# Performance work log

Measured on AMD Instinct MI355X. Metric: run time of the kernel, lower is better.

Reference implementation:

```python
import jax, jax.numpy as jnp
import numpy as np

HEADS = 16
D_MODEL = 1024
HEAD_DIM = D_MODEL // HEADS
NEG = -1e15


def setup_inputs() -> dict:
    key = jax.random.key(0)
    ks = jax.random.split(key, 13)
    B, L = 2, 2048
    scale = 1.0 / np.sqrt(D_MODEL)
    inp = {
        'q': jax.random.normal(ks[0], (B, L, D_MODEL), jnp.float32),
        'k': jax.random.normal(ks[1], (B, L, D_MODEL), jnp.float32),
        'v': jax.random.normal(ks[2], (B, L, D_MODEL), jnp.float32),
        'mask': jax.random.randint(ks[3], (B, 1, 1, L), 0, 2, jnp.int32),
        'Wq': jax.random.normal(ks[4], (D_MODEL, D_MODEL), jnp.float32) * scale,
        'bq': jax.random.normal(ks[5], (D_MODEL,), jnp.float32) * scale,
        'Wk': jax.random.normal(ks[6], (D_MODEL, D_MODEL), jnp.float32) * scale,
        'bk': jax.random.normal(ks[7], (D_MODEL,), jnp.float32) * scale,
        'Wv': jax.random.normal(ks[8], (D_MODEL, D_MODEL), jnp.float32) * scale,
        'bv': jax.random.normal(ks[9], (D_MODEL,), jnp.float32) * scale,
        'Wo': jax.random.normal(ks[10], (D_MODEL, D_MODEL), jnp.float32) * scale,
        'bo': jax.random.normal(ks[11], (D_MODEL,), jnp.float32) * scale,
    }
    return inp


def _split_heads(x):
    B, L, _ = x.shape
    return x.reshape(B, L, HEADS, HEAD_DIM).transpose(0, 2, 1, 3)  # [B,H,L,Dh]


def reference(q, k, v, mask, Wq, bq, Wk, bk, Wv, bv, Wo, bo):
    B, L, _ = q.shape
    # torch Linear: y = x @ W.T + b
    qh = _split_heads(q @ Wq.T + bq)
    kh = _split_heads(k @ Wk.T + bk)
    vh = _split_heads(v @ Wv.T + bv)
    scores = jnp.einsum('bhqd,bhkd->bhqk', qh, kh) / jnp.sqrt(jnp.float32(HEAD_DIM))
    scores = scores + mask.astype(scores.dtype) * NEG
    weights = jax.nn.softmax(scores, axis=-1)
    attn = jnp.einsum('bhqk,bhkd->bhqd', weights, vh)  # [B,H,L,Dh]
    attn = attn.transpose(0, 2, 1, 3).reshape(B, L, D_MODEL)
    return attn @ Wo.T + bo
```

## Files before the change

kernel.cpp:

```cpp
#include <hip/hip_runtime.h>
#include <stdint.h>

typedef __bf16 bf16;
typedef __attribute__((ext_vector_type(8))) __bf16 bf16x8;
typedef __attribute__((ext_vector_type(4))) __bf16 bf16x4;
typedef __attribute__((ext_vector_type(4))) float f32x4;

#define SEQ   2048
#define DM    1024
#define NH    16
#define HD    64
#define MROWS 4096

__device__ __forceinline__ void glds16(const bf16* g, bf16* l) {
  __builtin_amdgcn_global_load_lds(
      (__attribute__((address_space(1))) unsigned int*)(g),
      (__attribute__((address_space(3))) unsigned int*)(l),
      16, 0, 0);
}

static __device__ __forceinline__ bf16x8 cvt_f32x8(const float* __restrict__ p) {
  const f32x4 a = *(const f32x4*)p;
  const f32x4 b = *(const f32x4*)(p + 4);
  bf16x8 r;
  r[0] = (bf16)a[0]; r[1] = (bf16)a[1]; r[2] = (bf16)a[2]; r[3] = (bf16)a[3];
  r[4] = (bf16)b[0]; r[5] = (bf16)b[1]; r[6] = (bf16)b[2]; r[7] = (bf16)b[3];
  return r;
}

__global__ void conv_all(
    const float* __restrict__ q, const float* __restrict__ k, const float* __restrict__ v,
    const float* __restrict__ wq, const float* __restrict__ wk,
    const float* __restrict__ wv, const float* __restrict__ wo,
    bf16* __restrict__ dq, bf16* __restrict__ dk, bf16* __restrict__ dv,
    bf16* __restrict__ dwq, bf16* __restrict__ dwk, bf16* __restrict__ dwv,
    bf16* __restrict__ dwo)
{
  const size_t c = (size_t)blockIdx.x * 256 + threadIdx.x;
  const float* s; bf16* d; size_t off;
  if (c < 524288)        { s = q;  d = dq;  off = c; }
  else if (c < 1048576)  { s = k;  d = dk;  off = c - 524288; }
  else if (c < 1572864)  { s = v;  d = dv;  off = c - 1048576; }
  else if (c < 1703936)  { s = wq; d = dwq; off = c - 1572864; }
  else if (c < 1835008)  { s = wk; d = dwk; off = c - 1703936; }
  else if (c < 1966080)  { s = wv; d = dwv; off = c - 1835008; }
  else                   { s = wo; d = dwo; off = c - 1966080; }
  *(bf16x8*)(d + off * 8) = cvt_f32x8(s + off * 8);
}

__global__ __launch_bounds__(256, 4) void proj_qkv(
    const bf16* __restrict__ qb, const bf16* __restrict__ kb, const bf16* __restrict__ vb,
    const bf16* __restrict__ Wqb, const bf16* __restrict__ Wkb, const bf16* __restrict__ Wvb,
    const float* __restrict__ bq, const float* __restrict__ bk, const float* __restrict__ bv,
    bf16* __restrict__ Qh, bf16* __restrict__ Kh, bf16* __restrict__ Vt)
{
  __shared__ __align__(16) bf16 sA[128 * 64];
  __shared__ __align__(16) bf16 sB[128 * 64];

  const int z = blockIdx.z;
  const int o = (int)blockIdx.x + 8 * (int)blockIdx.y;
  const int rt = (o & 7) * 4 + ((o >> 3) & 3);
  const int ot = o >> 5;

  const bf16 *A, *B;
  const float* Bv;
  int m0, n0;
  if (z == 0)      { A = qb;  B = Wqb; Bv = bq; m0 = rt * 128; n0 = ot * 128; }
  else if (z == 1) { A = kb;  B = Wkb; Bv = bk; m0 = rt * 128; n0 = ot * 128; }
  else             { A = Wvb; B = vb;  Bv = bv; m0 = ot * 128; n0 = rt * 128; }

  const int tid  = threadIdx.x;
  const int lane = tid & 63;
  const int wv   = tid >> 6;
  const int quad = lane >> 4;
  const int colx = lane & 15;
  const int rm = (wv >> 1) * 64;
  const int rn = (wv & 1) * 64;

  f32x4 acc[4][4];
#pragma unroll
  for (int mi = 0; mi < 4; ++mi)
#pragma unroll
    for (int ni = 0; ni < 4; ++ni) {
      f32x4 zz = {0.f, 0.f, 0.f, 0.f};
      acc[mi][ni] = zz;
    }

  for (int kt = 0; kt < 16; ++kt) {
    const int k0 = kt * 64;
    __syncthreads();
#pragma unroll
    for (int i = 0; i < 4; ++i) {
      const int f = i * 256 + tid;
      const int row = f >> 3;
      const int cc = (f & 7) ^ (row & 7);
      glds16(A + (size_t)(m0 + row) * DM + k0 + cc * 8, sA + f * 8);
      glds16(B + (size_t)(n0 + row) * DM + k0 + cc * 8, sB + f * 8);
    }
    __syncthreads();

    bf16x8 af[4][2], bfr[4][2];
#pragma unroll
    for (int t4 = 0; t4 < 4; ++t4) {
#pragma unroll
      for (int ks = 0; ks < 2; ++ks) {
        const int ra = rm + t4 * 16 + colx;
        af[t4][ks] = *(const bf16x8*)(sA + ra * 64 + (((ks * 4 + quad) ^ (ra & 7)) * 8));
        const int rb = rn + t4 * 16 + colx;
        bfr[t4][ks] = *(const bf16x8*)(sB + rb * 64 + (((ks * 4 + quad) ^ (rb & 7)) * 8));
      }
    }
#pragma unroll
    for (int mi = 0; mi < 4; ++mi)
#pragma unroll
      for (int ni = 0; ni < 4; ++ni) {
        acc[mi][ni] = __builtin_amdgcn_mfma_f32_16x16x32_bf16(af[mi][0], bfr[ni][0], acc[mi][ni], 0, 0, 0);
        acc[mi][ni] = __builtin_amdgcn_mfma_f32_16x16x32_bf16(af[mi][1], bfr[ni][1], acc[mi][ni], 0, 0, 0);
      }
  }

  if (z == 2) {
#pragma unroll
    for (int mi = 0; mi < 4; ++mi) {
#pragma unroll
      for (int r = 0; r < 4; ++r) {
        const int m = m0 + rm + mi * 16 + quad * 4 + r;
        const float bias = Bv[m];
        const int hh = m >> 6, d = m & 63;
#pragma unroll
        for (int ni = 0; ni < 4; ++ni) {
          const int n = n0 + rn + ni * 16 + colx;
          const int b = n >> 11, l = n & 2047;
          const int lb = l >> 6, li = l & 63;
          const int perm = (li & 15) * 4 + ((li >> 4) & 3);
          Vt[(((size_t)(b * NH + hh) * HD + d) * SEQ) + lb * 64 + perm] =
              (bf16)(acc[mi][ni][r] + bias);
        }
      }
    }
  } else {
    bf16* Out = (z == 0) ? Qh : Kh;
    const float scale = (z == 0) ? 0.18033688f : 1.0f;
#pragma unroll
    for (int ni = 0; ni < 4; ++ni) {
      const int n = n0 + rn + ni * 16 + colx;
      const float bias = Bv[n];
#pragma unroll
      for (int mi = 0; mi < 4; ++mi) {
#pragma unroll
        for (int r = 0; r < 4; ++r) {
          const int m = m0 + rm + mi * 16 + quad * 4 + r;
          const float v = (acc[mi][ni][r] + bias) * scale;
          const int b = m >> 11, l = m & 2047, hh = n >> 6, d = n & 63;
          Out[((size_t)(b * NH + hh) * SEQ + l) * HD + d] = (bf16)v;
        }
      }
    }
  }
}

__global__ __launch_bounds__(256, 4) void proj_out(
    const bf16* __restrict__ At, const bf16* __restrict__ Wob,
    const float* __restrict__ bo, float* __restrict__ Out)
{
  __shared__ __align__(16) bf16 sA[128 * 64];
  __shared__ __align__(16) bf16 sB[128 * 64];

  const int o = (int)blockIdx.x + 8 * (int)blockIdx.y;
  const int m0 = ((o & 7) * 4 + ((o >> 3) & 3)) * 128;
  const int n0 = (o >> 5) * 128;

  const int tid  = threadIdx.x;
  const int lane = tid & 63;
  const int wv   = tid >> 6;
  const int quad = lane >> 4;
  const int colx = lane & 15;
  const int rm = (wv >> 1) * 64;
  const int rn = (wv & 1) * 64;

  f32x4 acc[4][4];
#pragma unroll
  for (int mi = 0; mi < 4; ++mi)
#pragma unroll
    for (int ni = 0; ni < 4; ++ni) {
      f32x4 zz = {0.f, 0.f, 0.f, 0.f};
      acc[mi][ni] = zz;
    }

  for (int kt = 0; kt < 16; ++kt) {
    const int k0 = kt * 64;
    __syncthreads();
#pragma unroll
    for (int i = 0; i < 4; ++i) {
      const int f = i * 256 + tid;
      const int row = f >> 3;
      const int cc = (f & 7) ^ (row & 7);
      glds16(At  + (size_t)(m0 + row) * DM + k0 + cc * 8, sA + f * 8);
      glds16(Wob + (size_t)(n0 + row) * DM + k0 + cc * 8, sB + f * 8);
    }
    __syncthreads();

    bf16x8 af[4][2], bfr[4][2];
#pragma unroll
    for (int t4 = 0; t4 < 4; ++t4) {
#pragma unroll
      for (int ks = 0; ks < 2; ++ks) {
        const int ra = rm + t4 * 16 + colx;
        af[t4][ks] = *(const bf16x8*)(sA + ra * 64 + (((ks * 4 + quad) ^ (ra & 7)) * 8));
        const int rb = rn + t4 * 16 + colx;
        bfr[t4][ks] = *(const bf16x8*)(sB + rb * 64 + (((ks * 4 + quad) ^ (rb & 7)) * 8));
      }
    }
#pragma unroll
    for (int mi = 0; mi < 4; ++mi)
#pragma unroll
      for (int ni = 0; ni < 4; ++ni) {
        acc[mi][ni] = __builtin_amdgcn_mfma_f32_16x16x32_bf16(af[mi][0], bfr[ni][0], acc[mi][ni], 0, 0, 0);
        acc[mi][ni] = __builtin_amdgcn_mfma_f32_16x16x32_bf16(af[mi][1], bfr[ni][1], acc[mi][ni], 0, 0, 0);
      }
  }

#pragma unroll
  for (int ni = 0; ni < 4; ++ni) {
    const int n = n0 + rn + ni * 16 + colx;
    const float bias = bo[n];
#pragma unroll
    for (int mi = 0; mi < 4; ++mi) {
#pragma unroll
      for (int r = 0; r < 4; ++r) {
        const int m = m0 + rm + mi * 16 + quad * 4 + r;
        Out[(size_t)m * DM + n] = acc[mi][ni][r] + bias;
      }
    }
  }
}

__global__ __launch_bounds__(256, 4) void attn_kernel(
    const bf16* __restrict__ Qh, const bf16* __restrict__ Kh, const bf16* __restrict__ Vt,
    const int* __restrict__ mask, bf16* __restrict__ At)
{
  __shared__ __align__(16) bf16 sK[2][64 * 64];
  __shared__ __align__(16) bf16 sV[2][64 * 64];
  __shared__ __align__(16) bf16 sP[4][16 * 64];

  const int tid  = threadIdx.x;
  const int lane = tid & 63;
  const int wv   = tid >> 6;
  const int quad = lane >> 4;
  const int colx = lane & 15;
  const int bh = blockIdx.x;
  const int b  = bh >> 4;
  const int h  = bh & 15;
  const int q0 = blockIdx.y * 64;
  const size_t base  = (size_t)bh * SEQ * HD;
  const size_t baseV = (size_t)bh * HD * SEQ;

  auto issue = [&](int K0, bf16* dK, bf16* dV) {
#pragma unroll
    for (int i = 0; i < 2; ++i) {
      const int f = i * 256 + tid;
      const int kr = f >> 3;
      const int ck = (f & 7) ^ (kr & 7);
      glds16(Kh + base + (size_t)(K0 + kr) * HD + ck * 8, dK + f * 8);
      const int dr = f >> 3;
      const int cv = (f & 7) ^ (dr & 7);
      glds16(Vt + baseV + (size_t)dr * SEQ + K0 + cv * 8, dV + f * 8);
    }
  };

  int mk[4];
  issue(0, sK[0], sV[0]);
#pragma unroll
  for (int nt = 0; nt < 4; ++nt)
    mk[nt] = mask[b * SEQ + nt * 16 + colx];

  bf16x8 qf[2];
  {
    const int qrow = q0 + wv * 16 + colx;
    qf[0] = *(const bf16x8*)(Qh + base + (size_t)qrow * HD + quad * 8);
    qf[1] = *(const bf16x8*)(Qh + base + (size_t)qrow * HD + 32 + quad * 8);
  }

  f32x4 o[4];
  float osum[4];
#pragma unroll
  for (int dt = 0; dt < 4; ++dt) {
    f32x4 zz = {0.f, 0.f, 0.f, 0.f};
    o[dt] = zz;
    osum[dt] = 0.f;
  }
  bf16* sPw = &sP[wv][0];

  __syncthreads();

  for (int kc = 0; kc < 32; ++kc) {
    const int cur = kc & 1;
    bf16* cK = &sK[cur][0];
    bf16* cV = &sV[cur][0];

    float mreg[4];
#pragma unroll
    for (int nt = 0; nt < 4; ++nt)
      mreg[nt] = (mk[nt] ? -1e30f : 0.0f) - 23.0830917f;

    if (kc < 31) {
      issue((kc + 1) * 64, &sK[cur ^ 1][0], &sV[cur ^ 1][0]);
#pragma unroll
      for (int nt = 0; nt < 4; ++nt)
        mk[nt] = mask[b * SEQ + (kc + 1) * 64 + nt * 16 + colx];
    }

    f32x4 s8[4];
#pragma unroll
    for (int nt = 0; nt < 4; ++nt) {
      f32x4 zz = {0.f, 0.f, 0.f, 0.f};
      s8[nt] = zz;
    }
    __builtin_amdgcn_s_setprio(1);
#pragma unroll
    for (int nt = 0; nt < 4; ++nt) {
      const int krow = nt * 16 + colx;
#pragma unroll
      for (int ks = 0; ks < 2; ++ks) {
        const bf16x8 kf = *(const bf16x8*)(cK + krow * 64 + (((ks * 4 + quad) ^ (krow & 7)) * 8));
        s8[nt] = __builtin_amdgcn_mfma_f32_16x16x32_bf16(qf[ks], kf, s8[nt], 0, 0, 0);
      }
    }
    __builtin_amdgcn_s_setprio(0);

    bf16x8 vf[2][4];
#pragma unroll
    for (int ks = 0; ks < 2; ++ks) {
#pragma unroll
      for (int dt = 0; dt < 4; ++dt) {
        const int row = dt * 16 + colx;
        vf[ks][dt] = *(const bf16x8*)(cV + row * 64 + (((ks * 4 + quad) ^ (row & 7)) * 8));
      }
    }

#pragma unroll
    for (int r = 0; r < 4; ++r) {
      bf16x4 pk;
      float rsum = 0.f;
#pragma unroll
      for (int nt = 0; nt < 4; ++nt) {
        const float e = __builtin_amdgcn_exp2f(s8[nt][r] + mreg[nt]);
        pk[nt] = (bf16)e;
        rsum += e;
      }
      const int row = quad * 4 + r;
      *(bf16x4*)(sPw + row * 64 + (((colx >> 1) ^ (row & 7)) * 8) + (colx & 1) * 4) = pk;
      osum[r] += rsum;
    }

    __builtin_amdgcn_s_setprio(1);
#pragma unroll
    for (int ks = 0; ks < 2; ++ks) {
      const bf16x8 pf = *(const bf16x8*)(sPw + colx * 64 + (((ks * 4 + quad) ^ (colx & 7)) * 8));
#pragma unroll
      for (int dt = 0; dt < 4; ++dt)
        o[dt] = __builtin_amdgcn_mfma_f32_16x16x32_bf16(pf, vf[ks][dt], o[dt], 0, 0, 0);
    }
    __builtin_amdgcn_s_setprio(0);

    __syncthreads();
  }

#pragma unroll
  for (int r = 0; r < 4; ++r) {
    float s = osum[r];
    s += __shfl_xor(s, 1);
    s += __shfl_xor(s, 2);
    s += __shfl_xor(s, 4);
    s += __shfl_xor(s, 8);
    const float inv = 1.0f / s;
    const int q = q0 + wv * 16 + quad * 4 + r;
#pragma unroll
    for (int dt = 0; dt < 4; ++dt) {
      At[((size_t)(b * SEQ + q)) * DM + h * HD + dt * 16 + colx] =
          (bf16)(o[dt][r] * inv);
    }
  }
}

extern "C" void kernel_launch(void* const* d_in, const int* in_sizes, int n_in,
                              void* d_out, int out_size, void* d_ws, size_t ws_size,
                              hipStream_t stream) {
  (void)in_sizes; (void)n_in; (void)out_size; (void)ws_size;
  const float* q    = (const float*)d_in[0];
  const float* k    = (const float*)d_in[1];
  const float* v    = (const float*)d_in[2];
  const int*   mask = (const int*)d_in[3];
  const float* Wq   = (const float*)d_in[4];
  const float* bq   = (const float*)d_in[5];
  const float* Wk   = (const float*)d_in[6];
  const float* bk   = (const float*)d_in[7];
  const float* Wv   = (const float*)d_in[8];
  const float* bv   = (const float*)d_in[9];
  const float* Wo   = (const float*)d_in[10];
  const float* bo   = (const float*)d_in[11];
  float* out = (float*)d_out;

  const size_t T = (size_t)MROWS * DM;
  const size_t WT = (size_t)DM * DM;
  bf16* ws  = (bf16*)d_ws;
  bf16* qb  = ws;
  bf16* kb  = qb + T;
  bf16* vb  = kb + T;
  bf16* Wqb = vb + T;
  bf16* Wkb = Wqb + WT;
  bf16* Wvb = Wkb + WT;
  bf16* Wob = Wvb + WT;
  bf16* Qh  = Wob + WT;
  bf16* Kh  = Qh + T;
  bf16* Vt  = Kh + T;
  bf16* At  = qb;

  dim3 blk(256);
  conv_all<<<8192, blk, 0, stream>>>(q, k, v, Wq, Wk, Wv, Wo,
                                     qb, kb, vb, Wqb, Wkb, Wvb, Wob);
  proj_qkv<<<dim3(8, 32, 3), blk, 0, stream>>>(qb, kb, vb, Wqb, Wkb, Wvb,
                                               bq, bk, bv, Qh, Kh, Vt);
  attn_kernel<<<dim3(32, 32), blk, 0, stream>>>(Qh, Kh, Vt, mask, At);
  proj_out<<<dim3(8, 32), blk, 0, stream>>>(At, Wob, bo, out);
}
```

Before: 217.2 us.

## Split attention keys across waves and reduce partial outputs through LDS

Rewrites the attention kernel so that each wave handles all 64 queries of the block but only a quarter of the keys. K, V and mask are loaded directly from global memory into registers instead of through double-buffered LDS, and S is computed transposed (K as the A operand) so the P fragment feeds the PV MFMA directly, with no P round trip through LDS. The V projection stores plain row-major Vt, dropping the old permutation. Partial outputs and denominators are combined serially across the four waves in LDS at the end. In exchange the kernel uses more accumulator registers, lowering the occupancy hint from 4 to 3, and loses LDS-based data sharing between waves.

```diff
diff --git a/kernel.cpp b/kernel.cpp
--- a/kernel.cpp
+++ b/kernel.cpp
@@ -131,9 +131,7 @@
         for (int ni = 0; ni < 4; ++ni) {
           const int n = n0 + rn + ni * 16 + colx;
           const int b = n >> 11, l = n & 2047;
-          const int lb = l >> 6, li = l & 63;
-          const int perm = (li & 15) * 4 + ((li >> 4) & 3);
-          Vt[(((size_t)(b * NH + hh) * HD + d) * SEQ) + lb * 64 + perm] =
+          Vt[(((size_t)(b * NH + hh) * HD + d) * SEQ) + l] =
               (bf16)(acc[mi][ni][r] + bias);
         }
       }
@@ -235,13 +233,12 @@
   }
 }
 
-__global__ __launch_bounds__(256, 4) void attn_kernel(
+__global__ __launch_bounds__(256, 3) void attn_kernel(
     const bf16* __restrict__ Qh, const bf16* __restrict__ Kh, const bf16* __restrict__ Vt,
     const int* __restrict__ mask, bf16* __restrict__ At)
 {
-  __shared__ __align__(16) bf16 sK[2][64 * 64];
-  __shared__ __align__(16) bf16 sV[2][64 * 64];
-  __shared__ __align__(16) bf16 sP[4][16 * 64];
+  __shared__ __align__(16) float sRed[64 * 68];
+  __shared__ float sDen[64];
 
   const int tid  = threadIdx.x;
   const int lane = tid & 63;
@@ -255,132 +252,134 @@
   const size_t base  = (size_t)bh * SEQ * HD;
   const size_t baseV = (size_t)bh * HD * SEQ;
 
-  auto issue = [&](int K0, bf16* dK, bf16* dV) {
-#pragma unroll
-    for (int i = 0; i < 2; ++i) {
-      const int f = i * 256 + tid;
-      const int kr = f >> 3;
-      const int ck = (f & 7) ^ (kr & 7);
-      glds16(Kh + base + (size_t)(K0 + kr) * HD + ck * 8, dK + f * 8);
-      const int dr = f >> 3;
-      const int cv = (f & 7) ^ (dr & 7);
-      glds16(Vt + baseV + (size_t)dr * SEQ + K0 + cv * 8, dV + f * 8);
-    }
-  };
-
-  int mk[4];
-  issue(0, sK[0], sV[0]);
-#pragma unroll
-  for (int nt = 0; nt < 4; ++nt)
-    mk[nt] = mask[b * SEQ + nt * 16 + colx];
-
-  bf16x8 qf[2];
-  {
-    const int qrow = q0 + wv * 16 + colx;
-    qf[0] = *(const bf16x8*)(Qh + base + (size_t)qrow * HD + quad * 8);
-    qf[1] = *(const bf16x8*)(Qh + base + (size_t)qrow * HD + 32 + quad * 8);
-  }
-
-  f32x4 o[4];
+  bf16x8 qf[4][2];
+#pragma unroll
+  for (int qg = 0; qg < 4; ++qg) {
+    const int qrow = q0 + qg * 16 + colx;
+    qf[qg][0] = *(const bf16x8*)(Qh + base + (size_t)qrow * HD + quad * 8);
+    qf[qg][1] = *(const bf16x8*)(Qh + base + (size_t)qrow * HD + 32 + quad * 8);
+  }
+
+  f32x4 o[4][4];
   float osum[4];
 #pragma unroll
-  for (int dt = 0; dt < 4; ++dt) {
-    f32x4 zz = {0.f, 0.f, 0.f, 0.f};
-    o[dt] = zz;
-    osum[dt] = 0.f;
-  }
-  bf16* sPw = &sP[wv][0];
-
-  __syncthreads();
-
-  for (int kc = 0; kc < 32; ++kc) {
-    const int cur = kc & 1;
-    bf16* cK = &sK[cur][0];
-    bf16* cV = &sV[cur][0];
-
-    float mreg[4];
-#pragma unroll
-    for (int nt = 0; nt < 4; ++nt)
-      mreg[nt] = (mk[nt] ? -1e30f : 0.0f) - 23.0830917f;
-
-    if (kc < 31) {
-      issue((kc + 1) * 64, &sK[cur ^ 1][0], &sV[cur ^ 1][0]);
-#pragma unroll
-      for (int nt = 0; nt < 4; ++nt)
-        mk[nt] = mask[b * SEQ + (kc + 1) * 64 + nt * 16 + colx];
-    }
-
-    f32x4 s8[4];
-#pragma unroll
-    for (int nt = 0; nt < 4; ++nt) {
+  for (int qg = 0; qg < 4; ++qg) {
+    osum[qg] = 0.f;
+#pragma unroll
+    for (int dt = 0; dt < 4; ++dt) {
       f32x4 zz = {0.f, 0.f, 0.f, 0.f};
-      s8[nt] = zz;
-    }
+      o[qg][dt] = zz;
+    }
+  }
+
+  union VV { bf16x8 v8; bf16x4 v4[2]; };
+
+  for (int t = 0; t < 16; ++t) {
+    const int kb = t * 128 + wv * 32;
+
+    bf16x8 kf[2][2];
+#pragma unroll
+    for (int g = 0; g < 2; ++g) {
+#pragma unroll
+      for (int ks = 0; ks < 2; ++ks)
+        kf[g][ks] = *(const bf16x8*)(Kh + base + (size_t)(kb + g * 16 + colx) * HD + ks * 32 + quad * 8);
+    }
+    const int4 m0 = *(const int4*)(mask + b * SEQ + kb + quad * 4);
+    const int4 m1 = *(const int4*)(mask + b * SEQ + kb + 16 + quad * 4);
+    VV vvp[4];
+#pragma unroll
+    for (int dt = 0; dt < 4; ++dt) {
+      const bf16* vrow = Vt + baseV + (size_t)(dt * 16 + colx) * SEQ + kb + quad * 4;
+      vvp[dt].v4[0] = *(const bf16x4*)(vrow);
+      vvp[dt].v4[1] = *(const bf16x4*)(vrow + 16);
+    }
+
+    float mr0[4], mr1[4];
+    mr0[0] = (m0.x ? -1e30f : 0.0f) - 23.0830917f;
+    mr0[1] = (m0.y ? -1e30f : 0.0f) - 23.0830917f;
+    mr0[2] = (m0.z ? -1e30f : 0.0f) - 23.0830917f;
+    mr0[3] = (m0.w ? -1e30f : 0.0f) - 23.0830917f;
+    mr1[0] = (m1.x ? -1e30f : 0.0f) - 23.0830917f;
+    mr1[1] = (m1.y ? -1e30f : 0.0f) - 23.0830917f;
+    mr1[2] = (m1.z ? -1e30f : 0.0f) - 23.0830917f;
+    mr1[3] = (m1.w ? -1e30f : 0.0f) - 23.0830917f;
+
+    VV pa[4];
     __builtin_amdgcn_s_setprio(1);
 #pragma unroll
-    for (int nt = 0; nt < 4; ++nt) {
-      const int krow = nt * 16 + colx;
-#pragma unroll
-      for (int ks = 0; ks < 2; ++ks) {
-        const bf16x8 kf = *(const bf16x8*)(cK + krow * 64 + (((ks * 4 + quad) ^ (krow & 7)) * 8));
-        s8[nt] = __builtin_amdgcn_mfma_f32_16x16x32_bf16(qf[ks], kf, s8[nt], 0, 0, 0);
-      }
+    for (int qg = 0; qg < 4; ++qg) {
+      f32x4 s = {0.f, 0.f, 0.f, 0.f};
+      s = __builtin_amdgcn_mfma_f32_16x16x32_bf16(kf[0][0], qf[qg][0], s, 0, 0, 0);
+      s = __builtin_amdgcn_mfma_f32_16x16x32_bf16(kf[0][1], qf[qg][1], s, 0, 0, 0);
+#pragma unroll
+      for (int r = 0; r < 4; ++r) {
+        const float e = __builtin_amdgcn_exp2f(s[r] + mr0[r]);
+        pa[qg].v8[r] = (bf16)e;
+        osum[qg] += e;
+      }
+    }
+#pragma unroll
+    for (int qg = 0; qg < 4; ++qg) {
+      f32x4 s = {0.f, 0.f, 0.f, 0.f};
+      s = __builtin_amdgcn_mfma_f32_16x16x32_bf16(kf[1][0], qf[qg][0], s, 0, 0, 0);
+      s = __builtin_amdgcn_mfma_f32_16x16x32_bf16(kf[1][1], qf[qg][1], s, 0, 0, 0);
+#pragma unroll
+      for (int r = 0; r < 4; ++r) {
+        const float e = __builtin_amdgcn_exp2f(s[r] + mr1[r]);
+        pa[qg].v8[4 + r] = (bf16)e;
+        osum[qg] += e;
+      }
+    }
+
+#pragma unroll
+    for (int dt = 0; dt < 4; ++dt) {
+#pragma unroll
+      for (int qg = 0; qg < 4; ++qg)
+        o[qg][dt] = __builtin_amdgcn_mfma_f32_16x16x32_bf16(pa[qg].v8, vvp[dt].v8, o[qg][dt], 0, 0, 0);
     }
     __builtin_amdgcn_s_setprio(0);
-
-    bf16x8 vf[2][4];
-#pragma unroll
-    for (int ks = 0; ks < 2; ++ks) {
-#pragma unroll
-      for (int dt = 0; dt < 4; ++dt) {
-        const int row = dt * 16 + colx;
-        vf[ks][dt] = *(const bf16x8*)(cV + row * 64 + (((ks * 4 + quad) ^ (row & 7)) * 8));
-      }
-    }
-
-#pragma unroll
-    for (int r = 0; r < 4; ++r) {
-      bf16x4 pk;
-      float rsum = 0.f;
-#pragma unroll
-      for (int nt = 0; nt < 4; ++nt) {
-        const float e = __builtin_amdgcn_exp2f(s8[nt][r] + mreg[nt]);
-        pk[nt] = (bf16)e;
-        rsum += e;
-      }
-      const int row = quad * 4 + r;
-      *(bf16x4*)(sPw + row * 64 + (((colx >> 1) ^ (row & 7)) * 8) + (colx & 1) * 4) = pk;
-      osum[r] += rsum;
-    }
-
-    __builtin_amdgcn_s_setprio(1);
-#pragma unroll
-    for (int ks = 0; ks < 2; ++ks) {
-      const bf16x8 pf = *(const bf16x8*)(sPw + colx * 64 + (((ks * 4 + quad) ^ (colx & 7)) * 8));
-#pragma unroll
-      for (int dt = 0; dt < 4; ++dt)
-        o[dt] = __builtin_amdgcn_mfma_f32_16x16x32_bf16(pf, vf[ks][dt], o[dt], 0, 0, 0);
-    }
-    __builtin_amdgcn_s_setprio(0);
-
+  }
+
+#pragma unroll
+  for (int qg = 0; qg < 4; ++qg) {
+    osum[qg] += __shfl_xor(osum[qg], 16);
+    osum[qg] += __shfl_xor(osum[qg], 32);
+  }
+  const float myden = (quad == 0) ? osum[0] : (quad == 1) ? osum[1]
+                    : (quad == 2) ? osum[2] : osum[3];
+
+#pragma unroll
+  for (int p = 0; p < 4; ++p) {
+    if (wv == p) {
+#pragma unroll
+      for (int qg = 0; qg < 4; ++qg)
+#pragma unroll
+        for (int dt = 0; dt < 4; ++dt) {
+          float* a = &sRed[(dt * 16 + colx) * 68 + qg * 16 + quad * 4];
+          if (p == 0) {
+            *(f32x4*)a = o[qg][dt];
+          } else {
+            f32x4 c = *(const f32x4*)a;
+            c += o[qg][dt];
+            *(f32x4*)a = c;
+          }
+        }
+      if (p == 0) sDen[quad * 16 + colx] = myden;
+      else        sDen[quad * 16 + colx] += myden;
+    }
     __syncthreads();
   }
 
-#pragma unroll
-  for (int r = 0; r < 4; ++r) {
-    float s = osum[r];
-    s += __shfl_xor(s, 1);
-    s += __shfl_xor(s, 2);
-    s += __shfl_xor(s, 4);
-    s += __shfl_xor(s, 8);
-    const float inv = 1.0f / s;
-    const int q = q0 + wv * 16 + quad * 4 + r;
-#pragma unroll
-    for (int dt = 0; dt < 4; ++dt) {
-      At[((size_t)(b * SEQ + q)) * DM + h * HD + dt * 16 + colx] =
-          (bf16)(o[dt][r] * inv);
-    }
-  }
+  const float inv = 1.0f / sDen[wv * 16 + colx];
+  bf16x8 out0, out1;
+#pragma unroll
+  for (int j = 0; j < 8; ++j) {
+    out0[j] = (bf16)(sRed[(quad * 16 + j) * 68 + wv * 16 + colx] * inv);
+    out1[j] = (bf16)(sRed[(quad * 16 + 8 + j) * 68 + wv * 16 + colx] * inv);
+  }
+  const size_t orow = ((size_t)(b * SEQ + q0 + wv * 16 + colx)) * DM + h * HD + quad * 16;
+  *(bf16x8*)(At + orow) = out0;
+  *(bf16x8*)(At + orow + 8) = out1;
 }
 
 extern "C" void kernel_launch(void* const* d_in, const int* in_sizes, int n_in,
```

Result: slower. 259.6 us (+19.5%).
